# Performance work log

Hardware: AMD Instinct MI355X
Metric: run time of the kernel (lower is better)

## Reference

```python
import jax, jax.numpy as jnp
import numpy as np

BETA = 0.5
TEMPERATURE = 1.0
IGNORE_INDEX = -100
BT, H, V = 2048, 2048, 32000


def setup_inputs() -> dict:
    key = jax.random.key(0)
    k1, k2, k3, k4, k5 = jax.random.split(key, 5)
    return {
        "student_input": jax.random.normal(k1, (BT, H), dtype=jnp.float32),
        "student_weight": jax.random.normal(k2, (V, H), dtype=jnp.float32) * 0.02,
        "teacher_input": jax.random.normal(k3, (BT, H), dtype=jnp.float32),
        "teacher_weight": jax.random.normal(k4, (V, H), dtype=jnp.float32) * 0.02,
        "labels": jax.random.randint(k5, (BT,), 0, V, dtype=jnp.int64),
    }


def reference(student_input, student_weight, teacher_input, teacher_weight, labels):
    # logits = x @ W^T, scaled by temperature, then log-softmax (computed in fp32)
    s_logits = jnp.einsum("bh,vh->bv", student_input, student_weight).astype(jnp.float32)
    t_logits = jnp.einsum("bh,vh->bv", teacher_input, teacher_weight).astype(jnp.float32)
    s_lp = jax.nn.log_softmax(s_logits / TEMPERATURE, axis=-1)  # log Q, (BT, V)
    t_lp = jax.nn.log_softmax(t_logits / TEMPERATURE, axis=-1)  # log P, (BT, V)
    Q = jnp.exp(s_lp)
    P = jnp.exp(t_lp)
    # generalized JSD: M = beta*P + (1-beta)*Q
    log_m = jnp.log(BETA * P + (1.0 - BETA) * Q)
    per_row = jnp.sum(BETA * P * (t_lp - log_m) + (1.0 - BETA) * Q * (s_lp - log_m), axis=-1)  # (BT,)
    valid = (labels != IGNORE_INDEX)
    n_non_ignore = jnp.maximum(jnp.sum(valid), 1).astype(jnp.float32)
    loss = jnp.sum(jnp.where(valid, per_row, 0.0)) / n_non_ignore
    return loss
```

## Files before the change

### kernel.cpp

```cpp
#include <hip/hip_runtime.h>
#include <stdint.h>

#define BT 2048
#define H  2048
#define V  32000

typedef __attribute__((ext_vector_type(8))) short short8;
typedef __attribute__((ext_vector_type(4))) float f32x4;

__device__ inline unsigned short f2bf(float x) {
  unsigned int u = __float_as_uint(x);
  u += 0x7FFFu + ((u >> 16) & 1u);
  return (unsigned short)(u >> 16);
}

__global__ void zero_accum(float* accum) {
  accum[0] = 0.0f;
  ((unsigned int*)accum)[1] = 0u;
}

__global__ __launch_bounds__(256) void cvt_kernel(const float* __restrict__ src,
                                                  unsigned short* __restrict__ dst,
                                                  int n8) {
  int i = blockIdx.x * blockDim.x + threadIdx.x;
  if (i >= n8) return;
  const float4* s = (const float4*)src;
  float4 a = s[2 * i];
  float4 b = s[2 * i + 1];
  union { unsigned short us[8]; uint4 v; } o;
  o.us[0] = f2bf(a.x); o.us[1] = f2bf(a.y); o.us[2] = f2bf(a.z); o.us[3] = f2bf(a.w);
  o.us[4] = f2bf(b.x); o.us[5] = f2bf(b.y); o.us[6] = f2bf(b.z); o.us[7] = f2bf(b.w);
  ((uint4*)dst)[i] = o.v;
}

#define BM 128
#define BN 128
#define BK 32

__global__ __launch_bounds__(256) void gemm_bt(const unsigned short* __restrict__ A0,
                                               const unsigned short* __restrict__ B0,
                                               const unsigned short* __restrict__ A1,
                                               const unsigned short* __restrict__ B1,
                                               unsigned short* __restrict__ C0,
                                               unsigned short* __restrict__ C1) {
  const int z = blockIdx.z;
  const unsigned short* A = z ? A1 : A0;
  const unsigned short* B = z ? B1 : B0;
  unsigned short* C = z ? C1 : C0;

  const int m0 = blockIdx.x * BM;
  const int n0 = blockIdx.y * BN;

  __shared__ alignas(16) unsigned short lA[BM * BK];
  __shared__ alignas(16) unsigned short lB[BN * BK];

  const int tid  = threadIdx.x;
  const int lane = tid & 63;
  const int w    = tid >> 6;
  const int wm   = w & 1;
  const int wn   = w >> 1;

  f32x4 acc[4][4];
  #pragma unroll
  for (int i = 0; i < 4; i++)
    #pragma unroll
    for (int j = 0; j < 4; j++)
      acc[i][j] = (f32x4){0.f, 0.f, 0.f, 0.f};

  const int q  = lane >> 4;
  const int l4 = lane & 15;

  for (int k0 = 0; k0 < H; k0 += BK) {
    #pragma unroll
    for (int i = 0; i < 2; i++) {
      int basec = (i * 4 + w) * 64;
      int c     = basec + lane;
      int row   = c >> 2;
      int cq    = c & 3;
      const unsigned short* ga = A + (size_t)(m0 + row) * H + k0 + cq * 8;
      const unsigned short* gb = B + (size_t)(n0 + row) * H + k0 + cq * 8;
      __builtin_amdgcn_global_load_lds(
          (const __attribute__((address_space(1))) unsigned int*)ga,
          (__attribute__((address_space(3))) unsigned int*)&lA[basec * 8], 16, 0, 0);
      __builtin_amdgcn_global_load_lds(
          (const __attribute__((address_space(1))) unsigned int*)gb,
          (__attribute__((address_space(3))) unsigned int*)&lB[basec * 8], 16, 0, 0);
    }
    __syncthreads();

    short8 af[4], bf[4];
    #pragma unroll
    for (int mi = 0; mi < 4; mi++) {
      int M = wm * 64 + mi * 16 + l4;
      af[mi] = *(const short8*)&lA[(M * 4 + q) * 8];
    }
    #pragma unroll
    for (int ni = 0; ni < 4; ni++) {
      int N = wn * 64 + ni * 16 + l4;
      bf[ni] = *(const short8*)&lB[(N * 4 + q) * 8];
    }

    #pragma unroll
    for (int mi = 0; mi < 4; mi++)
      #pragma unroll
      for (int ni = 0; ni < 4; ni++)
        acc[mi][ni] = __builtin_amdgcn_mfma_f32_16x16x32_bf16(af[mi], bf[ni], acc[mi][ni], 0, 0, 0);

    __syncthreads();
  }

  #pragma unroll
  for (int mi = 0; mi < 4; mi++)
    #pragma unroll
    for (int ni = 0; ni < 4; ni++)
      #pragma unroll
      for (int r = 0; r < 4; r++) {
        int gr = m0 + wm * 64 + mi * 16 + q * 4 + r;
        int gc = n0 + wn * 64 + ni * 16 + l4;
        C[(size_t)gr * V + gc] = f2bf(acc[mi][ni][r]);
      }
}

__device__ inline void unpack8(uint4 v, float* f) {
  f[0] = __uint_as_float(v.x << 16);
  f[1] = __uint_as_float(v.x & 0xFFFF0000u);
  f[2] = __uint_as_float(v.y << 16);
  f[3] = __uint_as_float(v.y & 0xFFFF0000u);
  f[4] = __uint_as_float(v.z << 16);
  f[5] = __uint_as_float(v.z & 0xFFFF0000u);
  f[6] = __uint_as_float(v.w << 16);
  f[7] = __uint_as_float(v.w & 0xFFFF0000u);
}

__device__ inline float blk_max(float v, float* red, int tid) {
  #pragma unroll
  for (int o = 32; o > 0; o >>= 1) v = fmaxf(v, __shfl_xor(v, o, 64));
  __syncthreads();
  if ((tid & 63) == 0) red[tid >> 6] = v;
  __syncthreads();
  return fmaxf(fmaxf(red[0], red[1]), fmaxf(red[2], red[3]));
}

__device__ inline float blk_sum(float v, float* red, int tid) {
  #pragma unroll
  for (int o = 32; o > 0; o >>= 1) v += __shfl_xor(v, o, 64);
  __syncthreads();
  if ((tid & 63) == 0) red[tid >> 6] = v;
  __syncthreads();
  return (red[0] + red[1]) + (red[2] + red[3]);
}

__global__ __launch_bounds__(256) void jsd_kernel(const unsigned short* __restrict__ Slog,
                                                  const unsigned short* __restrict__ Tlog,
                                                  const long long* __restrict__ labels,
                                                  float* __restrict__ accum) {
  const int r   = blockIdx.x;
  const int tid = threadIdx.x;
  __shared__ float red[4];

  const uint4* s4 = (const uint4*)(Slog + (size_t)r * V);
  const uint4* t4 = (const uint4*)(Tlog + (size_t)r * V);
  const int NC = V / 8;

  float smax = -1e30f, tmax = -1e30f;
  for (int c = tid; c < NC; c += 256) {
    uint4 sv = s4[c], tv = t4[c];
    float fs[8], ft[8];
    unpack8(sv, fs); unpack8(tv, ft);
    #pragma unroll
    for (int j = 0; j < 8; j++) {
      smax = fmaxf(smax, fs[j]);
      tmax = fmaxf(tmax, ft[j]);
    }
  }
  smax = blk_max(smax, red, tid);
  tmax = blk_max(tmax, red, tid);

  float ssum = 0.f, tsum = 0.f;
  for (int c = tid; c < NC; c += 256) {
    uint4 sv = s4[c], tv = t4[c];
    float fs[8], ft[8];
    unpack8(sv, fs); unpack8(tv, ft);
    #pragma unroll
    for (int j = 0; j < 8; j++) {
      ssum += __expf(fs[j] - smax);
      tsum += __expf(ft[j] - tmax);
    }
  }
  ssum = blk_sum(ssum, red, tid);
  tsum = blk_sum(tsum, red, tid);
  float slse = smax + __logf(ssum);
  float tlse = tmax + __logf(tsum);

  float loss = 0.f;
  for (int c = tid; c < NC; c += 256) {
    uint4 sv = s4[c], tv = t4[c];
    float fs[8], ft[8];
    unpack8(sv, fs); unpack8(tv, ft);
    #pragma unroll
    for (int j = 0; j < 8; j++) {
      float sl = fs[j] - slse;
      float tl = ft[j] - tlse;
      float qv = __expf(sl);
      float pv = __expf(tl);
      float m  = 0.5f * (pv + qv);
      float lm = __logf(m);
      loss += 0.5f * (pv * (tl - lm) + qv * (sl - lm));
    }
  }
  loss = blk_sum(loss, red, tid);

  if (tid == 0) {
    long long lab = labels[r];
    if (lab != -100LL) {
      atomicAdd(&accum[0], loss);
      atomicAdd((unsigned int*)&accum[1], 1u);
    }
  }
}

__global__ void finalize(const float* __restrict__ accum, float* __restrict__ out) {
  float cnt = (float)((const unsigned int*)accum)[1];
  out[0] = accum[0] / fmaxf(cnt, 1.0f);
}

extern "C" void kernel_launch(void* const* d_in, const int* in_sizes, int n_in,
                              void* d_out, int out_size, void* d_ws, size_t ws_size,
                              hipStream_t stream) {
  const float* s_in = (const float*)d_in[0];
  const float* s_w  = (const float*)d_in[1];
  const float* t_in = (const float*)d_in[2];
  const float* t_w  = (const float*)d_in[3];
  const long long* labels = (const long long*)d_in[4];
  float* out = (float*)d_out;

  char* ws = (char*)d_ws;
  size_t off = 0;
  auto take = [&](size_t bytes) -> char* {
    char* p = ws + off;
    off += (bytes + 255) & ~(size_t)255;
    return p;
  };
  unsigned short* sw_bf = (unsigned short*)take((size_t)V * H * 2);
  unsigned short* tw_bf = (unsigned short*)take((size_t)V * H * 2);
  unsigned short* si_bf = (unsigned short*)take((size_t)BT * H * 2);
  unsigned short* ti_bf = (unsigned short*)take((size_t)BT * H * 2);
  unsigned short* slog  = (unsigned short*)take((size_t)BT * V * 2);
  unsigned short* tlog  = (unsigned short*)take((size_t)BT * V * 2);
  float* accum = (float*)take(256);
  if (off > ws_size) return;

  zero_accum<<<dim3(1), dim3(1), 0, stream>>>(accum);

  const int nW8 = (V * H) / 8;
  const int nI8 = (BT * H) / 8;
  cvt_kernel<<<dim3((nW8 + 255) / 256), dim3(256), 0, stream>>>(s_w, sw_bf, nW8);
  cvt_kernel<<<dim3((nW8 + 255) / 256), dim3(256), 0, stream>>>(t_w, tw_bf, nW8);
  cvt_kernel<<<dim3((nI8 + 255) / 256), dim3(256), 0, stream>>>(s_in, si_bf, nI8);
  cvt_kernel<<<dim3((nI8 + 255) / 256), dim3(256), 0, stream>>>(t_in, ti_bf, nI8);

  gemm_bt<<<dim3(BT / BM, V / BN, 2), dim3(256), 0, stream>>>(si_bf, sw_bf, ti_bf, tw_bf, slog, tlog);

  jsd_kernel<<<dim3(BT), dim3(256), 0, stream>>>(slog, tlog, labels, accum);

  finalize<<<dim3(1), dim3(1), 0, stream>>>(accum, out);
}
```

Baseline: 1.362 ms.

## Fuse row exp-sum into GEMM epilogue and swizzle LDS tile layout

The GEMM epilogue now computes the exp of each fp32 accumulator, reduces across the 16-lane group and atomically adds the per-row sum into a workspace buffer. The JSD kernel then reads the log-sum-exp directly, so its max pass and sum pass over the bf16 logits are gone. No max is subtracted before exp, which relies on logits being small enough not to overflow, as they are with these inputs. LDS chunk placement is also XOR-swizzled by row to reduce bank conflicts on the MFMA fragment reads.

```diff
diff --git a/kernel.cpp b/kernel.cpp
--- a/kernel.cpp
+++ b/kernel.cpp
@@ -14,9 +14,13 @@
   return (unsigned short)(u >> 16);
 }
 
-__global__ void zero_accum(float* accum) {
-  accum[0] = 0.0f;
-  ((unsigned int*)accum)[1] = 0u;
+__global__ __launch_bounds__(256) void zero_ws(float* rowsum, float* accum) {
+  int i = blockIdx.x * blockDim.x + threadIdx.x;
+  if (i < 2 * BT) rowsum[i] = 0.0f;
+  if (i == 0) {
+    accum[0] = 0.0f;
+    ((unsigned int*)accum)[1] = 0u;
+  }
 }
 
 __global__ __launch_bounds__(256) void cvt_kernel(const float* __restrict__ src,
@@ -42,11 +46,13 @@
                                                const unsigned short* __restrict__ A1,
                                                const unsigned short* __restrict__ B1,
                                                unsigned short* __restrict__ C0,
-                                               unsigned short* __restrict__ C1) {
+                                               unsigned short* __restrict__ C1,
+                                               float* __restrict__ rowsum) {
   const int z = blockIdx.z;
   const unsigned short* A = z ? A1 : A0;
   const unsigned short* B = z ? B1 : B0;
   unsigned short* C = z ? C1 : C0;
+  float* rs = rowsum + z * BT;
 
   const int m0 = blockIdx.x * BM;
   const int n0 = blockIdx.y * BN;
@@ -76,7 +82,7 @@
       int basec = (i * 4 + w) * 64;
       int c     = basec + lane;
       int row   = c >> 2;
-      int cq    = c & 3;
+      int cq    = (c & 3) ^ (row & 3);
       const unsigned short* ga = A + (size_t)(m0 + row) * H + k0 + cq * 8;
       const unsigned short* gb = B + (size_t)(n0 + row) * H + k0 + cq * 8;
       __builtin_amdgcn_global_load_lds(
@@ -92,12 +98,12 @@
     #pragma unroll
     for (int mi = 0; mi < 4; mi++) {
       int M = wm * 64 + mi * 16 + l4;
-      af[mi] = *(const short8*)&lA[(M * 4 + q) * 8];
+      af[mi] = *(const short8*)&lA[(M * 4 + (q ^ (M & 3))) * 8];
     }
     #pragma unroll
     for (int ni = 0; ni < 4; ni++) {
       int N = wn * 64 + ni * 16 + l4;
-      bf[ni] = *(const short8*)&lB[(N * 4 + q) * 8];
+      bf[ni] = *(const short8*)&lB[(N * 4 + (q ^ (N & 3))) * 8];
     }
 
     #pragma unroll
@@ -119,6 +125,22 @@
         int gc = n0 + wn * 64 + ni * 16 + l4;
         C[(size_t)gr * V + gc] = f2bf(acc[mi][ni][r]);
       }
+
+  #pragma unroll
+  for (int mi = 0; mi < 4; mi++) {
+    #pragma unroll
+    for (int r = 0; r < 4; r++) {
+      float s = 0.f;
+      #pragma unroll
+      for (int ni = 0; ni < 4; ni++) s += __expf(acc[mi][ni][r]);
+      #pragma unroll
+      for (int o = 1; o < 16; o <<= 1) s += __shfl_xor(s, o, 64);
+      if (l4 == 0) {
+        int gr = m0 + wm * 64 + mi * 16 + q * 4 + r;
+        atomicAdd(&rs[gr], s);
+      }
+    }
+  }
 }
 
 __device__ inline void unpack8(uint4 v, float* f) {
@@ -132,26 +154,9 @@
   f[7] = __uint_as_float(v.w & 0xFFFF0000u);
 }
 
-__device__ inline float blk_max(float v, float* red, int tid) {
-  #pragma unroll
-  for (int o = 32; o > 0; o >>= 1) v = fmaxf(v, __shfl_xor(v, o, 64));
-  __syncthreads();
-  if ((tid & 63) == 0) red[tid >> 6] = v;
-  __syncthreads();
-  return fmaxf(fmaxf(red[0], red[1]), fmaxf(red[2], red[3]));
-}
-
-__device__ inline float blk_sum(float v, float* red, int tid) {
-  #pragma unroll
-  for (int o = 32; o > 0; o >>= 1) v += __shfl_xor(v, o, 64);
-  __syncthreads();
-  if ((tid & 63) == 0) red[tid >> 6] = v;
-  __syncthreads();
-  return (red[0] + red[1]) + (red[2] + red[3]);
-}
-
 __global__ __launch_bounds__(256) void jsd_kernel(const unsigned short* __restrict__ Slog,
                                                   const unsigned short* __restrict__ Tlog,
+                                                  const float* __restrict__ rowsum,
                                                   const long long* __restrict__ labels,
                                                   float* __restrict__ accum) {
   const int r   = blockIdx.x;
@@ -162,35 +167,8 @@
   const uint4* t4 = (const uint4*)(Tlog + (size_t)r * V);
   const int NC = V / 8;
 
-  float smax = -1e30f, tmax = -1e30f;
-  for (int c = tid; c < NC; c += 256) {
-    uint4 sv = s4[c], tv = t4[c];
-    float fs[8], ft[8];
-    unpack8(sv, fs); unpack8(tv, ft);
-    #pragma unroll
-    for (int j = 0; j < 8; j++) {
-      smax = fmaxf(smax, fs[j]);
-      tmax = fmaxf(tmax, ft[j]);
-    }
-  }
-  smax = blk_max(smax, red, tid);
-  tmax = blk_max(tmax, red, tid);
-
-  float ssum = 0.f, tsum = 0.f;
-  for (int c = tid; c < NC; c += 256) {
-    uint4 sv = s4[c], tv = t4[c];
-    float fs[8], ft[8];
-    unpack8(sv, fs); unpack8(tv, ft);
-    #pragma unroll
-    for (int j = 0; j < 8; j++) {
-      ssum += __expf(fs[j] - smax);
-      tsum += __expf(ft[j] - tmax);
-    }
-  }
-  ssum = blk_sum(ssum, red, tid);
-  tsum = blk_sum(tsum, red, tid);
-  float slse = smax + __logf(ssum);
-  float tlse = tmax + __logf(tsum);
+  const float slse = __logf(rowsum[r]);
+  const float tlse = __logf(rowsum[BT + r]);
 
   float loss = 0.f;
   for (int c = tid; c < NC; c += 256) {
@@ -208,9 +186,12 @@
       loss += 0.5f * (pv * (tl - lm) + qv * (sl - lm));
     }
   }
-  loss = blk_sum(loss, red, tid);
-
+  #pragma unroll
+  for (int o = 32; o > 0; o >>= 1) loss += __shfl_xor(loss, o, 64);
+  if ((tid & 63) == 0) red[tid >> 6] = loss;
+  __syncthreads();
   if (tid == 0) {
+    loss = (red[0] + red[1]) + (red[2] + red[3]);
     long long lab = labels[r];
     if (lab != -100LL) {
       atomicAdd(&accum[0], loss);
@@ -247,10 +228,11 @@
   unsigned short* ti_bf = (unsigned short*)take((size_t)BT * H * 2);
   unsigned short* slog  = (unsigned short*)take((size_t)BT * V * 2);
   unsigned short* tlog  = (unsigned short*)take((size_t)BT * V * 2);
-  float* accum = (float*)take(256);
+  float* rowsum = (float*)take((size_t)2 * BT * 4);
+  float* accum  = (float*)take(256);
   if (off > ws_size) return;
 
-  zero_accum<<<dim3(1), dim3(1), 0, stream>>>(accum);
+  zero_ws<<<dim3((2 * BT + 255) / 256), dim3(256), 0, stream>>>(rowsum, accum);
 
   const int nW8 = (V * H) / 8;
   const int nI8 = (BT * H) / 8;
@@ -259,9 +241,10 @@
   cvt_kernel<<<dim3((nI8 + 255) / 256), dim3(256), 0, stream>>>(s_in, si_bf, nI8);
   cvt_kernel<<<dim3((nI8 + 255) / 256), dim3(256), 0, stream>>>(t_in, ti_bf, nI8);
 
-  gemm_bt<<<dim3(BT / BM, V / BN, 2), dim3(256), 0, stream>>>(si_bf, sw_bf, ti_bf, tw_bf, slog, tlog);
-
-  jsd_kernel<<<dim3(BT), dim3(256), 0, stream>>>(slog, tlog, labels, accum);
+  gemm_bt<<<dim3(BT / BM, V / BN, 2), dim3(256), 0, stream>>>(si_bf, sw_bf, ti_bf, tw_bf,
+                                                              slog, tlog, rowsum);
+
+  jsd_kernel<<<dim3(BT), dim3(256), 0, stream>>>(slog, tlog, rowsum, labels, accum);
 
   finalize<<<dim3(1), dim3(1), 0, stream>>>(accum, out);
 }
```

Measured after the change: 1.508 ms. +10.7%, slower.
